# Optimization experiments

Measured on AMD Instinct MI355X. Metric: run time of the kernel, lower is better.

The kernel has to match this reference:

```python
import jax, jax.numpy as jnp
import numpy as np

B, T, E, D, A, V, EMB = 256, 64, 2048, 512, 512, 10000, 256

def _glorot(key, shape):
    lim = np.sqrt(6.0 / (shape[0] + shape[-1]))
    return jax.random.uniform(key, shape, jnp.float32, -lim, lim)

def setup_inputs() -> dict:
    key = jax.random.key(0)
    ks = jax.random.split(key, 16)
    return {
        'input_c': jax.random.randint(ks[0], (B, 1), 0, V),
        'hidden': jax.random.normal(ks[1], (B, D), jnp.float32),
        'carry': jax.random.normal(ks[2], (B, D), jnp.float32),
        'encoder_output': jax.random.normal(ks[3], (B, T, E), jnp.float32),
        'emb': jax.random.normal(ks[4], (V, EMB), jnp.float32) * 0.05,
        'w1': _glorot(ks[5], (D, A)),  'b1': jnp.zeros((A,), jnp.float32),
        'w2': _glorot(ks[6], (E, A)),  'b2': jnp.zeros((A,), jnp.float32),
        'v':  _glorot(ks[7], (A, 1)),  'bv': jnp.zeros((1,), jnp.float32),
        'wx': _glorot(ks[8], (E + EMB, 4 * D)),
        'wh': _glorot(ks[9], (D, 4 * D)),
        'bl': jnp.zeros((4 * D,), jnp.float32),
        'wp': _glorot(ks[10], (D, V)), 'bp': jnp.zeros((V,), jnp.float32),
    }

def reference(input_c, hidden, carry, encoder_output, emb, w1, b1, w2, b2, v, bv, wx, wh, bl, wp, bp):
    # embedding: [B,1] -> [B,EMB] after squeeze
    x = emb[input_c[:, 0]]
    # Bahdanau additive attention: score = v^T tanh(W1 h + W2 enc)
    q = hidden @ w1 + b1                                # [B,A]
    k = jnp.einsum('bte,ea->bta', encoder_output, w2) + b2  # [B,T,A]
    score = jnp.tanh(q[:, None, :] + k) @ v + bv        # [B,T,1]
    attn = jax.nn.softmax(score, axis=1)                # [B,T,1]
    context = jnp.sum(attn * encoder_output, axis=1)    # [B,E]
    # LSTM cell (keras gate order i,f,c,o); dropout inactive (training=False)
    lstm_in = jnp.concatenate([context, x], axis=-1)    # [B,E+EMB]
    z = lstm_in @ wx + hidden @ wh + bl                 # [B,4D]
    i, f, g, o = jnp.split(z, 4, axis=-1)
    c_new = jax.nn.sigmoid(f) * carry + jax.nn.sigmoid(i) * jnp.tanh(g)
    h_new = jax.nn.sigmoid(o) * jnp.tanh(c_new)
    logits = h_new @ wp + bp                            # [B,V]
    return logits, h_new, c_new
```

## Files before the change

kernel.cpp:

```cpp
#include <hip/hip_runtime.h>
#include <hip/hip_bf16.h>
#include <math.h>

#define BB 256
#define TT 64
#define EE 2048
#define DD 512
#define AA 512
#define VV 10000
#define VPAD 10240
#define EMBD 256
#define KLSTM (EE + EMBD + DD)
#define N4D (4 * DD)
#define MROWS (BB * TT)

using bf16x8 = __attribute__((ext_vector_type(8))) __bf16;
using f32x4  = __attribute__((ext_vector_type(4))) float;

#define GLL16(gp, lp) __builtin_amdgcn_global_load_lds( \
    (const __attribute__((address_space(1))) void*)(gp), \
    (__attribute__((address_space(3))) void*)(lp), 16, 0, 0)

__device__ __forceinline__ float sigf(float x) { return 1.f / (1.f + expf(-x)); }

__global__ void k_q(const float* __restrict__ hidden, const float* __restrict__ w1,
                    const float* __restrict__ b1, const float* __restrict__ b2,
                    float* __restrict__ qq) {
    __shared__ float hs[DD];
    const int b = blockIdx.x, tid = threadIdx.x;
    {
        float2 hv = *(const float2*)&hidden[(size_t)b * DD + 2 * tid];
        hs[2 * tid] = hv.x; hs[2 * tid + 1] = hv.y;
    }
    __syncthreads();
    const int a0 = 2 * tid;
    float2 acc = {0.f, 0.f};
    #pragma unroll 4
    for (int k = 0; k < DD; ++k) {
        float2 w = *(const float2*)&w1[(size_t)k * AA + a0];
        float h = hs[k];
        acc.x = fmaf(h, w.x, acc.x);
        acc.y = fmaf(h, w.y, acc.y);
    }
    qq[(size_t)b * AA + a0]     = acc.x + b1[a0]     + b2[a0];
    qq[(size_t)b * AA + a0 + 1] = acc.y + b1[a0 + 1] + b2[a0 + 1];
}

__global__ void k_w2t(const float* __restrict__ w2, __bf16* __restrict__ w2t) {
    __shared__ float t[32][33];
    const int k0 = blockIdx.x * 32, n0 = blockIdx.y * 32;
    const int tx = threadIdx.x, ty = threadIdx.y;
    #pragma unroll
    for (int i = 0; i < 4; ++i)
        t[ty + 8 * i][tx] = w2[(size_t)(k0 + ty + 8 * i) * AA + n0 + tx];
    __syncthreads();
    #pragma unroll
    for (int i = 0; i < 4; ++i)
        w2t[(size_t)(n0 + ty + 8 * i) * EE + k0 + tx] = (__bf16)t[tx][ty + 8 * i];
}

__global__ void k_wxht(const float* __restrict__ wx, const float* __restrict__ wh,
                       __bf16* __restrict__ wt) {
    __shared__ float t[32][33];
    const int k0 = blockIdx.x * 32, n0 = blockIdx.y * 32;
    const int tx = threadIdx.x, ty = threadIdx.y;
    #pragma unroll
    for (int i = 0; i < 4; ++i) {
        int k = k0 + ty + 8 * i;
        const float* wrow = (k < EE + EMBD) ? &wx[(size_t)k * N4D] : &wh[(size_t)(k - EE - EMBD) * N4D];
        t[ty + 8 * i][tx] = wrow[n0 + tx];
    }
    __syncthreads();
    #pragma unroll
    for (int i = 0; i < 4; ++i)
        wt[(size_t)(n0 + ty + 8 * i) * KLSTM + k0 + tx] = (__bf16)t[tx][ty + 8 * i];
}

__global__ void k_wpt(const float* __restrict__ wp, __bf16* __restrict__ wpt) {
    __shared__ float t[32][33];
    const int k0 = blockIdx.x * 32, n0 = blockIdx.y * 32;
    const int tx = threadIdx.x, ty = threadIdx.y;
    #pragma unroll
    for (int i = 0; i < 4; ++i) {
        int n = n0 + tx;
        t[ty + 8 * i][tx] = wp[(size_t)(k0 + ty + 8 * i) * VV + (n < VV ? n : VV - 1)];
    }
    __syncthreads();
    #pragma unroll
    for (int i = 0; i < 4; ++i)
        wpt[(size_t)(n0 + ty + 8 * i) * DD + k0 + tx] = (__bf16)t[tx][ty + 8 * i];
}

__global__ __launch_bounds__(512, 2) void k_score(
        const float* __restrict__ enc, const __bf16* __restrict__ w2t,
        const float* __restrict__ qq, const float* __restrict__ vvec,
        float* __restrict__ spart) {
    __shared__ bf16x8 Abuf[128][8];
    __shared__ bf16x8 Bbuf[128][8];
    __shared__ float qsv[128], vsv[128], wredL[4][128];
    const int tid = threadIdx.x;
    const int mb = blockIdx.x & 127, nb = blockIdx.x >> 7;
    const int m0 = mb * 128, n0 = nb * 128;
    const int l = tid & 63, wv = tid >> 6;
    const int wm = wv >> 2, wn = wv & 3;
    const int ar = l & 15, agr = l >> 4;

    if (tid < 128) qsv[tid] = qq[(size_t)(2 * mb + 0) * 0 + 0], qsv[tid] = 0.f;
    __shared__ float qsv2[2][128];
    if (tid < 256) {
        int i = tid >> 7, col = tid & 127;
        qsv2[i][col] = qq[(size_t)(2 * mb + i) * AA + n0 + col];
    } else if (tid < 384) {
        vsv[tid - 256] = vvec[n0 + tid - 256];
    }

    const int arow = tid >> 2, ag0 = (tid & 3) * 2;
    const float* aptr = enc + (size_t)(m0 + arow) * EE + ag0 * 8;

    const int brow0 = wv * 16;
    const __bf16* bsrc = w2t + (size_t)(n0 + brow0 + (l >> 3)) * EE
                             + ((l & 7) ^ (l >> 3)) * 8;

    f32x4 acc[4][2];
    #pragma unroll
    for (int mi = 0; mi < 4; ++mi)
        #pragma unroll
        for (int ni = 0; ni < 2; ++ni)
            acc[mi][ni] = (f32x4){0.f, 0.f, 0.f, 0.f};

    const int NIT = EE / 64;
    for (int it = 0; it < NIT; ++it) {
        if (it > 0) __syncthreads();
        #pragma unroll
        for (int i = 0; i < 2; ++i)
            GLL16(bsrc + (size_t)i * 8 * EE + it * 64, &Bbuf[brow0 + i * 8][0]);
        {
            float4 u0 = *(const float4*)(aptr + it * 64);
            float4 u1 = *(const float4*)(aptr + it * 64 + 4);
            float4 u2 = *(const float4*)(aptr + it * 64 + 8);
            float4 u3 = *(const float4*)(aptr + it * 64 + 12);
            bf16x8 pk;
            pk[0] = (__bf16)u0.x; pk[1] = (__bf16)u0.y; pk[2] = (__bf16)u0.z; pk[3] = (__bf16)u0.w;
            pk[4] = (__bf16)u1.x; pk[5] = (__bf16)u1.y; pk[6] = (__bf16)u1.z; pk[7] = (__bf16)u1.w;
            Abuf[arow][ag0 ^ (arow & 7)] = pk;
            pk[0] = (__bf16)u2.x; pk[1] = (__bf16)u2.y; pk[2] = (__bf16)u2.z; pk[3] = (__bf16)u2.w;
            pk[4] = (__bf16)u3.x; pk[5] = (__bf16)u3.y; pk[6] = (__bf16)u3.z; pk[7] = (__bf16)u3.w;
            Abuf[arow][(ag0 + 1) ^ (arow & 7)] = pk;
        }
        __syncthreads();
        #pragma unroll
        for (int ks = 0; ks < 2; ++ks) {
            bf16x8 afr[4], bfr[2];
            #pragma unroll
            for (int mi = 0; mi < 4; ++mi)
                afr[mi] = Abuf[wm * 64 + mi * 16 + ar][(ks * 4 + agr) ^ (ar & 7)];
            #pragma unroll
            for (int ni = 0; ni < 2; ++ni)
                bfr[ni] = Bbuf[wn * 32 + ni * 16 + ar][(ks * 4 + agr) ^ (ar & 7)];
            #pragma unroll
            for (int mi = 0; mi < 4; ++mi)
                #pragma unroll
                for (int ni = 0; ni < 2; ++ni)
                    acc[mi][ni] = __builtin_amdgcn_mfma_f32_16x16x32_bf16(afr[mi], bfr[ni], acc[mi][ni], 0, 0, 0);
        }
    }

    float sred[4][4];
    #pragma unroll
    for (int mi = 0; mi < 4; ++mi)
        #pragma unroll
        for (int r = 0; r < 4; ++r) sred[mi][r] = 0.f;
    #pragma unroll
    for (int ni = 0; ni < 2; ++ni) {
        const int col = wn * 32 + ni * 16 + ar;
        const float va = vsv[col];
        const float qa = qsv2[wm][col];
        #pragma unroll
        for (int mi = 0; mi < 4; ++mi)
            #pragma unroll
            for (int r = 0; r < 4; ++r)
                sred[mi][r] += tanhf(qa + acc[mi][ni][r]) * va;
    }
    #pragma unroll
    for (int mi = 0; mi < 4; ++mi)
        #pragma unroll
        for (int r = 0; r < 4; ++r) {
            #pragma unroll
            for (int off = 1; off < 16; off <<= 1)
                sred[mi][r] += __shfl_xor(sred[mi][r], off, 64);
        }
    if (ar == 0) {
        #pragma unroll
        for (int mi = 0; mi < 4; ++mi)
            #pragma unroll
            for (int r = 0; r < 4; ++r)
                wredL[wn][wm * 64 + mi * 16 + agr * 4 + r] = sred[mi][r];
    }
    __syncthreads();
    if (tid < 128)
        spart[(size_t)nb * MROWS + m0 + tid] =
            wredL[0][tid] + wredL[1][tid] + wredL[2][tid] + wredL[3][tid];
}

__global__ void k_context(const float* __restrict__ enc, const float* __restrict__ spart,
                          const float* __restrict__ bv, float* __restrict__ ctx) {
    __shared__ float attn[TT];
    const int b = blockIdx.y;
    const int tid = threadIdx.x;
    if (tid < 64) {
        const int m = b * TT + tid;
        float s = spart[m] + spart[MROWS + m] + spart[2 * MROWS + m] + spart[3 * MROWS + m] + bv[0];
        float mx = s;
        #pragma unroll
        for (int off = 1; off < 64; off <<= 1) mx = fmaxf(mx, __shfl_xor(mx, off, 64));
        float p = expf(s - mx);
        float sum = p;
        #pragma unroll
        for (int off = 1; off < 64; off <<= 1) sum += __shfl_xor(sum, off, 64);
        attn[tid] = p / sum;
    }
    __syncthreads();
    const int e = blockIdx.x * 1024 + tid * 4;
    const float* encb = enc + (size_t)b * TT * EE + e;
    float4 acc = {0.f, 0.f, 0.f, 0.f};
    #pragma unroll 4
    for (int t = 0; t < TT; ++t) {
        float a = attn[t];
        float4 ev = *(const float4*)&encb[(size_t)t * EE];
        acc.x = fmaf(a, ev.x, acc.x);
        acc.y = fmaf(a, ev.y, acc.y);
        acc.z = fmaf(a, ev.z, acc.z);
        acc.w = fmaf(a, ev.w, acc.w);
    }
    *(float4*)&ctx[(size_t)b * EE + e] = acc;
}

#define ZKS 4
#define ZKC (KLSTM / ZKS)
#define ZNIT (ZKC / 32)
__global__ void k_z(const float* __restrict__ ctx, const float* __restrict__ emb,
                    const int* __restrict__ cidx, const float* __restrict__ hidden,
                    const __bf16* __restrict__ wt, float* __restrict__ zp) {
    __shared__ bf16x8 Abuf[32][ZKC / 8];
    __shared__ int cbs[32];
    const int tid = threadIdx.x;
    const int l = tid & 63, wv = tid >> 6;
    const int b0  = blockIdx.y * 32;
    const int kc0 = blockIdx.z * ZKC;
    const int nw  = blockIdx.x * 256 + wv * 64;

    if (tid < 32) cbs[tid] = cidx[b0 + tid];
    __syncthreads();

    {
        const int srow = tid >> 3, g0 = tid & 7;
        const int bg = b0 + srow;
        const int erow = cbs[srow];
        #pragma unroll
        for (int i = 0; i < 11; ++i) {
            int g = g0 + 8 * i;
            int k = kc0 + g * 8;
            const float* src;
            if (k < EE)             src = &ctx[(size_t)bg * EE + k];
            else if (k < EE + EMBD) src = &emb[(size_t)erow * EMBD + (k - EE)];
            else                    src = &hidden[(size_t)bg * DD + (k - EE - EMBD)];
            float4 u0 = *(const float4*)src;
            float4 u1 = *(const float4*)(src + 4);
            bf16x8 pk;
            pk[0] = (__bf16)u0.x; pk[1] = (__bf16)u0.y; pk[2] = (__bf16)u0.z; pk[3] = (__bf16)u0.w;
            pk[4] = (__bf16)u1.x; pk[5] = (__bf16)u1.y; pk[6] = (__bf16)u1.z; pk[7] = (__bf16)u1.w;
            Abuf[srow][g ^ (srow & 7)] = pk;
        }
    }
    __syncthreads();

    const int ar = l & 15, agr = l >> 4;
    const __bf16* bbase = wt + (size_t)(nw + ar) * KLSTM + kc0 + agr * 8;

    f32x4 acc[2][4];
    #pragma unroll
    for (int mt = 0; mt < 2; ++mt)
        #pragma unroll
        for (int f = 0; f < 4; ++f)
            acc[mt][f] = (f32x4){0.f, 0.f, 0.f, 0.f};

    bf16x8 bA[4], bBv[4];
    #pragma unroll
    for (int f = 0; f < 4; ++f)
        bA[f] = *(const bf16x8*)(bbase + (size_t)f * 16 * KLSTM);

    for (int itp = 0; itp < ZNIT / 2; ++itp) {
        const int it0 = 2 * itp, it1 = 2 * itp + 1;
        #pragma unroll
        for (int f = 0; f < 4; ++f)
            bBv[f] = *(const bf16x8*)(bbase + (size_t)f * 16 * KLSTM + it1 * 32);
        {
            bf16x8 a0 = Abuf[ar][(it0 * 4 + agr) ^ (ar & 7)];
            bf16x8 a1 = Abuf[16 + ar][(it0 * 4 + agr) ^ (ar & 7)];
            #pragma unroll
            for (int f = 0; f < 4; ++f) {
                acc[0][f] = __builtin_amdgcn_mfma_f32_16x16x32_bf16(a0, bA[f], acc[0][f], 0, 0, 0);
                acc[1][f] = __builtin_amdgcn_mfma_f32_16x16x32_bf16(a1, bA[f], acc[1][f], 0, 0, 0);
            }
        }
        const int it2 = (it1 + 1 < ZNIT) ? it1 + 1 : it1;
        #pragma unroll
        for (int f = 0; f < 4; ++f)
            bA[f] = *(const bf16x8*)(bbase + (size_t)f * 16 * KLSTM + it2 * 32);
        {
            bf16x8 a0 = Abuf[ar][(it1 * 4 + agr) ^ (ar & 7)];
            bf16x8 a1 = Abuf[16 + ar][(it1 * 4 + agr) ^ (ar & 7)];
            #pragma unroll
            for (int f = 0; f < 4; ++f) {
                acc[0][f] = __builtin_amdgcn_mfma_f32_16x16x32_bf16(a0, bBv[f], acc[0][f], 0, 0, 0);
                acc[1][f] = __builtin_amdgcn_mfma_f32_16x16x32_bf16(a1, bBv[f], acc[1][f], 0, 0, 0);
            }
        }
    }

    float* zpo = zp + (size_t)blockIdx.z * BB * N4D;
    #pragma unroll
    for (int mt = 0; mt < 2; ++mt)
        #pragma unroll
        for (int f = 0; f < 4; ++f)
            #pragma unroll
            for (int r = 0; r < 4; ++r)
                zpo[(size_t)(b0 + mt * 16 + agr * 4 + r) * N4D + nw + f * 16 + ar] = acc[mt][f][r];
}

__global__ void k_gates(const float* __restrict__ zp, const float* __restrict__ carry,
                        const float* __restrict__ bl,
                        float* __restrict__ hout, float* __restrict__ cout) {
    const int b = blockIdx.x, tid = threadIdx.x;
    const size_t P = (size_t)BB * N4D;
    #pragma unroll
    for (int r = 0; r < 2; ++r) {
        int d = tid + r * 256;
        float zi = bl[d], zf = bl[DD + d], zg = bl[2 * DD + d], zo = bl[3 * DD + d];
        #pragma unroll
        for (int ks = 0; ks < ZKS; ++ks) {
            const float* zb = zp + ks * P + (size_t)b * N4D;
            zi += zb[d];
            zf += zb[DD + d];
            zg += zb[2 * DD + d];
            zo += zb[3 * DD + d];
        }
        float c = carry[(size_t)b * DD + d];
        float cn = sigf(zf) * c + sigf(zi) * tanhf(zg);
        float hn = sigf(zo) * tanhf(cn);
        cout[(size_t)b * DD + d] = cn;
        hout[(size_t)b * DD + d] = hn;
    }
}

__global__ __launch_bounds__(256, 4) void k_logits(
        const float* __restrict__ hnew, const __bf16* __restrict__ wpt,
        const float* __restrict__ bp, float* __restrict__ logits) {
    __shared__ bf16x8 Abuf[64][8];
    __shared__ bf16x8 Bbuf[128][8];
    __shared__ float bps[128];
    const int tid = threadIdx.x;
    const int nb = blockIdx.x % 80, mb = blockIdx.x / 80;
    const int m0 = mb * 64, n0 = nb * 128;
    const int l = tid & 63, wv = tid >> 6;
    const int wm = wv >> 1, wn = wv & 1;
    const int ar = l & 15, agr = l >> 4;

    if (tid < 128) {
        int j = n0 + tid;
        bps[tid] = (j < VV) ? bp[j] : 0.f;
    }

    const int arow = tid >> 2, ag0 = (tid & 3) * 2;
    const float* aptr = hnew + (size_t)(m0 + arow) * DD + ag0 * 8;
    const int brow = tid >> 1, bg0 = (tid & 1) * 4;
    const __bf16* bptr = wpt + (size_t)(n0 + brow) * DD + bg0 * 8;

    f32x4 acc[2][4];
    #pragma unroll
    for (int mi = 0; mi < 2; ++mi)
        #pragma unroll
        for (int ni = 0; ni < 4; ++ni)
            acc[mi][ni] = (f32x4){0.f, 0.f, 0.f, 0.f};

    float4 af[4];
    bf16x8 bstg[4];
    #pragma unroll
    for (int j = 0; j < 4; ++j) af[j] = *(const float4*)(aptr + j * 4);
    #pragma unroll
    for (int i = 0; i < 4; ++i) bstg[i] = *(const bf16x8*)(bptr + i * 8);

    const int NIT = DD / 64;
    for (int it = 0; it < NIT; ++it) {
        if (it > 0) __syncthreads();
        {
            bf16x8 pk;
            pk[0] = (__bf16)af[0].x; pk[1] = (__bf16)af[0].y; pk[2] = (__bf16)af[0].z; pk[3] = (__bf16)af[0].w;
            pk[4] = (__bf16)af[1].x; pk[5] = (__bf16)af[1].y; pk[6] = (__bf16)af[1].z; pk[7] = (__bf16)af[1].w;
            Abuf[arow][ag0 ^ (arow & 7)] = pk;
            pk[0] = (__bf16)af[2].x; pk[1] = (__bf16)af[2].y; pk[2] = (__bf16)af[2].z; pk[3] = (__bf16)af[2].w;
            pk[4] = (__bf16)af[3].x; pk[5] = (__bf16)af[3].y; pk[6] = (__bf16)af[3].z; pk[7] = (__bf16)af[3].w;
            Abuf[arow][(ag0 + 1) ^ (arow & 7)] = pk;
        }
        #pragma unroll
        for (int i = 0; i < 4; ++i)
            Bbuf[brow][(bg0 + i) ^ (brow & 7)] = bstg[i];
        if (it + 1 < NIT) {
            const int k1 = (it + 1) * 64;
            #pragma unroll
            for (int j = 0; j < 4; ++j) af[j] = *(const float4*)(aptr + k1 + j * 4);
            #pragma unroll
            for (int i = 0; i < 4; ++i) bstg[i] = *(const bf16x8*)(bptr + k1 + i * 8);
        }
        __syncthreads();
        #pragma unroll
        for (int ks = 0; ks < 2; ++ks) {
            bf16x8 afr[2], bfr[4];
            #pragma unroll
            for (int mi = 0; mi < 2; ++mi)
                afr[mi] = Abuf[wm * 32 + mi * 16 + ar][(ks * 4 + agr) ^ (ar & 7)];
            #pragma unroll
            for (int ni = 0; ni < 4; ++ni)
                bfr[ni] = Bbuf[wn * 64 + ni * 16 + ar][(ks * 4 + agr) ^ (ar & 7)];
            #pragma unroll
            for (int mi = 0; mi < 2; ++mi)
                #pragma unroll
                for (int ni = 0; ni < 4; ++ni)
                    acc[mi][ni] = __builtin_amdgcn_mfma_f32_16x16x32_bf16(afr[mi], bfr[ni], acc[mi][ni], 0, 0, 0);
        }
    }

    #pragma unroll
    for (int mi = 0; mi < 2; ++mi)
        #pragma unroll
        for (int ni = 0; ni < 4; ++ni) {
            const int colL = wn * 64 + ni * 16 + ar;
            const int col = n0 + colL;
            if (col < VV) {
                const float bb = bps[colL];
                #pragma unroll
                for (int r = 0; r < 4; ++r) {
                    const int row = m0 + wm * 32 + mi * 16 + agr * 4 + r;
                    logits[(size_t)row * VV + col] = acc[mi][ni][r] + bb;
                }
            }
        }
}

extern "C" void kernel_launch(void* const* d_in, const int* in_sizes, int n_in,
                              void* d_out, int out_size, void* d_ws, size_t ws_size,
                              hipStream_t stream) {
    const int*   cidx   = (const int*)d_in[0];
    const float* hidden = (const float*)d_in[1];
    const float* carry  = (const float*)d_in[2];
    const float* enc    = (const float*)d_in[3];
    const float* emb    = (const float*)d_in[4];
    const float* w1     = (const float*)d_in[5];
    const float* b1     = (const float*)d_in[6];
    const float* w2     = (const float*)d_in[7];
    const float* b2     = (const float*)d_in[8];
    const float* vvec   = (const float*)d_in[9];
    const float* bv     = (const float*)d_in[10];
    const float* wx     = (const float*)d_in[11];
    const float* wh     = (const float*)d_in[12];
    const float* bl     = (const float*)d_in[13];
    const float* wp     = (const float*)d_in[14];
    const float* bp     = (const float*)d_in[15];

    float* out    = (float*)d_out;
    float* logits = out;
    float* hout   = out + (size_t)BB * VV;
    float* cout   = hout + (size_t)BB * DD;

    float* ws    = (float*)d_ws;
    float* qq    = ws;
    float* score = qq + (size_t)BB * AA;
    float* ctx   = score + (size_t)BB * TT;
    float* zp    = ctx + (size_t)BB * EE;
    __bf16* wxh_t = (__bf16*)(zp + (size_t)ZKS * BB * N4D);
    float* spart = (float*)(wxh_t + (size_t)N4D * KLSTM);
    __bf16* wpt  = (__bf16*)(spart + (size_t)4 * MROWS);
    __bf16* w2t  = (__bf16*)ctx;

    hipLaunchKernelGGL(k_w2t,     dim3(EE / 32, AA / 32),    dim3(32, 8), 0, stream, w2, w2t);
    hipLaunchKernelGGL(k_wxht,    dim3(KLSTM / 32, N4D / 32), dim3(32, 8), 0, stream, wx, wh, wxh_t);
    hipLaunchKernelGGL(k_wpt,     dim3(DD / 32, VPAD / 32),  dim3(32, 8), 0, stream, wp, wpt);
    hipLaunchKernelGGL(k_q,       dim3(BB),                  dim3(256), 0, stream, hidden, w1, b1, b2, qq);
    hipLaunchKernelGGL(k_score,   dim3(512),                 dim3(512), 0, stream, enc, w2t, qq, vvec, spart);
    hipLaunchKernelGGL(k_context, dim3(2, BB),               dim3(256), 0, stream, enc, spart, bv, ctx);
    hipLaunchKernelGGL(k_z,       dim3(N4D / 256, BB / 32, ZKS), dim3(256), 0, stream, ctx, emb, cidx, hidden, wxh_t, zp);
    hipLaunchKernelGGL(k_gates,   dim3(BB),                  dim3(256), 0, stream, zp, carry, bl, hout, cout);
    hipLaunchKernelGGL(k_logits,  dim3(320),                 dim3(256), 0, stream, hout, wpt, bp, logits);
}
```

Baseline: 190.5 us.

## Double-buffer score GEMM tiles and use 4 waves with larger per-wave tiles

The attention score GEMM kernel now uses double-buffered LDS tiles. The next K-slice of the encoder and W2 is prefetched, through registers and global_load_lds, while MFMAs run on the current slice, leaving one barrier per iteration instead of two. The block shrinks from 8 waves to 4, and each wave computes a 64x64 tile (4x4 MFMA accumulators), which improves operand reuse from LDS. The risks are higher register pressure and fewer waves per CU to hide latency.

```diff
diff --git a/kernel.cpp b/kernel.cpp
--- a/kernel.cpp
+++ b/kernel.cpp
@@ -91,78 +91,97 @@
         wpt[(size_t)(n0 + ty + 8 * i) * DD + k0 + tx] = (__bf16)t[tx][ty + 8 * i];
 }
 
-__global__ __launch_bounds__(512, 2) void k_score(
+__global__ __launch_bounds__(256, 2) void k_score(
         const float* __restrict__ enc, const __bf16* __restrict__ w2t,
         const float* __restrict__ qq, const float* __restrict__ vvec,
         float* __restrict__ spart) {
-    __shared__ bf16x8 Abuf[128][8];
-    __shared__ bf16x8 Bbuf[128][8];
-    __shared__ float qsv[128], vsv[128], wredL[4][128];
+    __shared__ bf16x8 Abuf[2][128][8];
+    __shared__ bf16x8 Bbuf[2][128][8];
+    __shared__ float qsv2[2][128], vsv[128], wredL[2][128];
     const int tid = threadIdx.x;
     const int mb = blockIdx.x & 127, nb = blockIdx.x >> 7;
     const int m0 = mb * 128, n0 = nb * 128;
     const int l = tid & 63, wv = tid >> 6;
-    const int wm = wv >> 2, wn = wv & 3;
+    const int wm = wv >> 1, wn = wv & 1;
     const int ar = l & 15, agr = l >> 4;
 
-    if (tid < 128) qsv[tid] = qq[(size_t)(2 * mb + 0) * 0 + 0], qsv[tid] = 0.f;
-    __shared__ float qsv2[2][128];
-    if (tid < 256) {
+    {
         int i = tid >> 7, col = tid & 127;
         qsv2[i][col] = qq[(size_t)(2 * mb + i) * AA + n0 + col];
-    } else if (tid < 384) {
-        vsv[tid - 256] = vvec[n0 + tid - 256];
-    }
-
-    const int arow = tid >> 2, ag0 = (tid & 3) * 2;
-    const float* aptr = enc + (size_t)(m0 + arow) * EE + ag0 * 8;
-
-    const int brow0 = wv * 16;
+        if (tid < 128) vsv[tid] = vvec[n0 + tid];
+    }
+
+    const int arow = tid >> 1, ahalf = tid & 1;
+    const float* aptr = enc + (size_t)(m0 + arow) * EE + ahalf * 32;
+
+    const int brow0 = wv * 32;
     const __bf16* bsrc = w2t + (size_t)(n0 + brow0 + (l >> 3)) * EE
                              + ((l & 7) ^ (l >> 3)) * 8;
 
-    f32x4 acc[4][2];
+    f32x4 acc[4][4];
     #pragma unroll
     for (int mi = 0; mi < 4; ++mi)
         #pragma unroll
-        for (int ni = 0; ni < 2; ++ni)
+        for (int ni = 0; ni < 4; ++ni)
             acc[mi][ni] = (f32x4){0.f, 0.f, 0.f, 0.f};
 
-    const int NIT = EE / 64;
-    for (int it = 0; it < NIT; ++it) {
-        if (it > 0) __syncthreads();
-        #pragma unroll
-        for (int i = 0; i < 2; ++i)
-            GLL16(bsrc + (size_t)i * 8 * EE + it * 64, &Bbuf[brow0 + i * 8][0]);
-        {
-            float4 u0 = *(const float4*)(aptr + it * 64);
-            float4 u1 = *(const float4*)(aptr + it * 64 + 4);
-            float4 u2 = *(const float4*)(aptr + it * 64 + 8);
-            float4 u3 = *(const float4*)(aptr + it * 64 + 12);
+    #pragma unroll
+    for (int i = 0; i < 4; ++i)
+        GLL16(bsrc + (size_t)i * 8 * EE, &Bbuf[0][brow0 + i * 8][0]);
+    {
+        #pragma unroll
+        for (int j = 0; j < 4; ++j) {
+            float4 u0 = *(const float4*)(aptr + j * 8);
+            float4 u1 = *(const float4*)(aptr + j * 8 + 4);
             bf16x8 pk;
             pk[0] = (__bf16)u0.x; pk[1] = (__bf16)u0.y; pk[2] = (__bf16)u0.z; pk[3] = (__bf16)u0.w;
             pk[4] = (__bf16)u1.x; pk[5] = (__bf16)u1.y; pk[6] = (__bf16)u1.z; pk[7] = (__bf16)u1.w;
-            Abuf[arow][ag0 ^ (arow & 7)] = pk;
-            pk[0] = (__bf16)u2.x; pk[1] = (__bf16)u2.y; pk[2] = (__bf16)u2.z; pk[3] = (__bf16)u2.w;
-            pk[4] = (__bf16)u3.x; pk[5] = (__bf16)u3.y; pk[6] = (__bf16)u3.z; pk[7] = (__bf16)u3.w;
-            Abuf[arow][(ag0 + 1) ^ (arow & 7)] = pk;
-        }
-        __syncthreads();
+            Abuf[0][arow][(ahalf * 4 + j) ^ (arow & 7)] = pk;
+        }
+    }
+    __syncthreads();
+
+    const int NIT = EE / 64;
+    for (int it = 0; it < NIT; ++it) {
+        const int cur = it & 1;
+        const bool more = (it + 1 < NIT);
+        float4 af[8];
+        if (more) {
+            const int k1 = (it + 1) * 64;
+            #pragma unroll
+            for (int i = 0; i < 4; ++i)
+                GLL16(bsrc + (size_t)i * 8 * EE + k1, &Bbuf[cur ^ 1][brow0 + i * 8][0]);
+            #pragma unroll
+            for (int j = 0; j < 8; ++j)
+                af[j] = *(const float4*)(aptr + k1 + j * 4);
+        }
         #pragma unroll
         for (int ks = 0; ks < 2; ++ks) {
-            bf16x8 afr[4], bfr[2];
+            bf16x8 afr[4], bfr[4];
             #pragma unroll
             for (int mi = 0; mi < 4; ++mi)
-                afr[mi] = Abuf[wm * 64 + mi * 16 + ar][(ks * 4 + agr) ^ (ar & 7)];
-            #pragma unroll
-            for (int ni = 0; ni < 2; ++ni)
-                bfr[ni] = Bbuf[wn * 32 + ni * 16 + ar][(ks * 4 + agr) ^ (ar & 7)];
+                afr[mi] = Abuf[cur][wm * 64 + mi * 16 + ar][(ks * 4 + agr) ^ (ar & 7)];
+            #pragma unroll
+            for (int ni = 0; ni < 4; ++ni)
+                bfr[ni] = Bbuf[cur][wn * 64 + ni * 16 + ar][(ks * 4 + agr) ^ (ar & 7)];
             #pragma unroll
             for (int mi = 0; mi < 4; ++mi)
                 #pragma unroll
-                for (int ni = 0; ni < 2; ++ni)
+                for (int ni = 0; ni < 4; ++ni)
                     acc[mi][ni] = __builtin_amdgcn_mfma_f32_16x16x32_bf16(afr[mi], bfr[ni], acc[mi][ni], 0, 0, 0);
         }
+        if (more) {
+            #pragma unroll
+            for (int j = 0; j < 4; ++j) {
+                bf16x8 pk;
+                pk[0] = (__bf16)af[2 * j].x;     pk[1] = (__bf16)af[2 * j].y;
+                pk[2] = (__bf16)af[2 * j].z;     pk[3] = (__bf16)af[2 * j].w;
+                pk[4] = (__bf16)af[2 * j + 1].x; pk[5] = (__bf16)af[2 * j + 1].y;
+                pk[6] = (__bf16)af[2 * j + 1].z; pk[7] = (__bf16)af[2 * j + 1].w;
+                Abuf[cur ^ 1][arow][(ahalf * 4 + j) ^ (arow & 7)] = pk;
+            }
+        }
+        __syncthreads();
     }
 
     float sred[4][4];
@@ -171,10 +190,9 @@
         #pragma unroll
         for (int r = 0; r < 4; ++r) sred[mi][r] = 0.f;
     #pragma unroll
-    for (int ni = 0; ni < 2; ++ni) {
-        const int col = wn * 32 + ni * 16 + ar;
-        const float va = vsv[col];
-        const float qa = qsv2[wm][col];
+    for (int ni = 0; ni < 4; ++ni) {
+        const int col = wn * 64 + ni * 16 + ar;
+        const float qa = qsv2[wm][col], va = vsv[col];
         #pragma unroll
         for (int mi = 0; mi < 4; ++mi)
             #pragma unroll
@@ -198,8 +216,7 @@
     }
     __syncthreads();
     if (tid < 128)
-        spart[(size_t)nb * MROWS + m0 + tid] =
-            wredL[0][tid] + wredL[1][tid] + wredL[2][tid] + wredL[3][tid];
+        spart[(size_t)nb * MROWS + m0 + tid] = wredL[0][tid] + wredL[1][tid];
 }
 
 __global__ void k_context(const float* __restrict__ enc, const float* __restrict__ spart,
@@ -486,7 +503,7 @@
     hipLaunchKernelGGL(k_wxht,    dim3(KLSTM / 32, N4D / 32), dim3(32, 8), 0, stream, wx, wh, wxh_t);
     hipLaunchKernelGGL(k_wpt,     dim3(DD / 32, VPAD / 32),  dim3(32, 8), 0, stream, wp, wpt);
     hipLaunchKernelGGL(k_q,       dim3(BB),                  dim3(256), 0, stream, hidden, w1, b1, b2, qq);
-    hipLaunchKernelGGL(k_score,   dim3(512),                 dim3(512), 0, stream, enc, w2t, qq, vvec, spart);
+    hipLaunchKernelGGL(k_score,   dim3(512),                 dim3(256), 0, stream, enc, w2t, qq, vvec, spart);
     hipLaunchKernelGGL(k_context, dim3(2, BB),               dim3(256), 0, stream, enc, spart, bv, ctx);
     hipLaunchKernelGGL(k_z,       dim3(N4D / 256, BB / 32, ZKS), dim3(256), 0, stream, ctx, emb, cidx, hidden, wxh_t, zp);
     hipLaunchKernelGGL(k_gates,   dim3(BB),                  dim3(256), 0, stream, zp, carry, bl, hout, cout);
```

New measurement: 219.5 us. +15.2%, slower.
